# Kernel tuning notes

Hardware: AMD Instinct MI355X
Metric: run time of the kernel (lower is better)

## Reference

```python
import jax, jax.numpy as jnp
import numpy as np

H = 1024   # hidden_size
S = 1024   # seq_length
B = 32     # batch_size


def setup_inputs() -> dict:
    key = jax.random.key(0)
    k1, k2, k3, k4, k5, k6 = jax.random.split(key, 6)
    scale = 1.0 / np.sqrt(3 * H)
    return {
        "encoder_states": jax.random.normal(k1, (S, B, 2 * H), dtype=jnp.float32),
        "hidden": jax.random.normal(k2, (B, H), dtype=jnp.float32),
        "cell": jax.random.normal(k3, (B, H), dtype=jnp.float32),
        "W_attn": jax.random.normal(k4, (H, 3 * H), dtype=jnp.float32) * scale,
        "b_attn": jax.random.normal(k5, (H,), dtype=jnp.float32) * scale,
        "v_w": jax.random.normal(k6, (H,), dtype=jnp.float32) * (1.0 / np.sqrt(H)),
    }


def reference(encoder_states, hidden, cell, W_attn, b_attn, v_w):
    # cell is accepted by the original forward but unused.
    # Split the concat-linear into two projections (mathematically identical,
    # avoids materializing the repeated hidden + concat tensor):
    # cat((hidden_rep, enc), -1) @ W.T == hidden @ W[:, :H].T + enc @ W[:, H:].T
    W_h = W_attn[:, :H]          # [H, H]   multiplies decoder hidden
    W_e = W_attn[:, H:]          # [H, 2H]  multiplies encoder states
    enc = jnp.transpose(encoder_states, (1, 0, 2))          # [B, S, 2H]
    h_proj = hidden @ W_h.T + b_attn                         # [B, H], broadcast over S
    e_proj = jnp.einsum("bse,he->bsh", enc, W_e)             # [B, S, H]
    energy = jnp.tanh(h_proj[:, None, :] + e_proj)           # [B, S, H]
    attention = jnp.einsum("bsh,h->bs", energy, v_w)         # [B, S]
    return jax.nn.softmax(attention, axis=1)
```

## Files before the change

### kernel.cpp

```cpp
#include <hip/hip_runtime.h>
#include <hip/hip_bf16.h>

#define H 1024
#define S 1024
#define B 32
#define K2 2048

typedef unsigned short u16;
typedef __attribute__((ext_vector_type(8))) short short8;
typedef __attribute__((ext_vector_type(8))) unsigned short u16x8;
typedef __attribute__((ext_vector_type(4))) float floatx4;

__device__ __forceinline__ u16 f2bf(float f) {
  unsigned u = __float_as_uint(f);
  u += 0x7FFFu + ((u >> 16) & 1u);
  return (u16)(u >> 16);
}

__device__ __forceinline__ void gld_lds16(const void* g, void* l) {
  __builtin_amdgcn_global_load_lds(
      (const __attribute__((address_space(1))) unsigned int*)g,
      (__attribute__((address_space(3))) unsigned int*)l, 16, 0, 0);
}

__device__ __forceinline__ unsigned cvt_pk(float lo, float hi) {
  __hip_bfloat162 h = __float22bfloat162_rn(float2{lo, hi});
  return *(unsigned*)&h;
}

__device__ __forceinline__ short8 mk_frag(floatx4 lo, floatx4 hi) {
  union { unsigned u[4]; short8 s; } r;
  r.u[0] = cvt_pk(lo[0], lo[1]);
  r.u[1] = cvt_pk(lo[2], lo[3]);
  r.u[2] = cvt_pk(hi[0], hi[1]);
  r.u[3] = cvt_pk(hi[2], hi[3]);
  return r.s;
}

__global__ void conv_we_k(const float* __restrict__ W, u16* __restrict__ dst) {
  const int h = blockIdx.x;
  const int t = threadIdx.x * 8;
  const float* sp = W + (size_t)h * 3072 + H + t;
  u16* dp = dst + (size_t)h * K2 + t;
  floatx4 x = *(const floatx4*)sp;
  floatx4 y = *(const floatx4*)(sp + 4);
  u16x8 o;
  o[0] = f2bf(x[0]); o[1] = f2bf(x[1]); o[2] = f2bf(x[2]); o[3] = f2bf(x[3]);
  o[4] = f2bf(y[0]); o[5] = f2bf(y[1]); o[6] = f2bf(y[2]); o[7] = f2bf(y[3]);
  *(u16x8*)dp = o;
}

__global__ void hproj_k(const float* __restrict__ hidden, const float* __restrict__ W,
                        const float* __restrict__ b_attn, float* __restrict__ hp) {
  const int lane = threadIdx.x & 63;
  const int h = (blockIdx.x * blockDim.x + threadIdx.x) >> 6;
  float wr[16];
#pragma unroll
  for (int i = 0; i < 16; i++) wr[i] = W[(size_t)h * 3072 + lane + i * 64];
  for (int b = 0; b < B; b++) {
    float d = 0.f;
#pragma unroll
    for (int i = 0; i < 16; i++) d = fmaf(wr[i], hidden[b * H + lane + i * 64], d);
#pragma unroll
    for (int off = 32; off; off >>= 1) d += __shfl_xor(d, off);
    if (lane == 0) hp[b * H + h] = d + b_attn[h];
  }
}

#define BM 128
#define BN 128
#define BK 32

__global__ __launch_bounds__(256) void gemm_fused_k(
    const float* __restrict__ enc,
    const u16* __restrict__ Bw,
    const float* __restrict__ hp, const float* __restrict__ vw,
    float* __restrict__ attn) {
  __shared__ __align__(16) float sA[BM * 32];
  __shared__ __align__(16) u16 sB[BN * BK];
  const int tid = threadIdx.x;
  const int bid = blockIdx.x;
  const int ntile = bid >> 8;
  const int b = (bid & 255) >> 3;
  const int mtile = bid & 7;
  const int s0 = mtile * BM;
  const int h0 = ntile * BN;

  const int lane = tid & 63;
  const int wv = tid >> 6;
  const int wm = (wv >> 1) * 64;
  const int wn = (wv & 1) * 64;
  const int fr = lane & 15;
  const int kgrp = lane >> 4;

  const int lr8 = lane >> 3, sg8 = lane & 7;
  const int lr4 = lane >> 2, sg4 = lane & 3;

  floatx4 acc[4][4];
#pragma unroll
  for (int i = 0; i < 4; i++)
#pragma unroll
    for (int j = 0; j < 4; j++) acc[i][j] = (floatx4){0.f, 0.f, 0.f, 0.f};

  for (int k0 = 0; k0 < K2; k0 += BK) {
    __syncthreads();
#pragma unroll
    for (int p = 0; p < 4; p++) {
      const int r = wv * 32 + p * 8 + lr8;
      gld_lds16(enc + ((size_t)(s0 + r) * B + b) * K2 + k0 + ((sg8 ^ (r & 7)) << 2),
                (char*)sA + (wv * 32 + p * 8) * 128);
    }
#pragma unroll
    for (int p = 0; p < 2; p++) {
      const int r = wv * 32 + p * 16 + lr4;
      gld_lds16(Bw + (size_t)(h0 + r) * K2 + k0 + ((sg4 ^ ((r >> 1) & 3)) << 3),
                (char*)sB + (wv * 32 + p * 16) * 64);
    }
    __syncthreads();

    short8 af[4], bf[4];
#pragma unroll
    for (int mf = 0; mf < 4; mf++) {
      const int R = wm + mf * 16 + fr;
      const int f7 = R & 7;
      floatx4 lo = *(const floatx4*)&sA[R * 32 + ((((kgrp << 1)) ^ f7) << 2)];
      floatx4 hi = *(const floatx4*)&sA[R * 32 + ((((kgrp << 1) | 1) ^ f7) << 2)];
      af[mf] = mk_frag(lo, hi);
    }
#pragma unroll
    for (int nf = 0; nf < 4; nf++) {
      const int R = wn + nf * 16 + fr;
      bf[nf] = *(const short8*)&sB[R * BK + ((kgrp ^ ((R >> 1) & 3)) << 3)];
    }
#pragma unroll
    for (int mf = 0; mf < 4; mf++)
#pragma unroll
      for (int nf = 0; nf < 4; nf++)
        acc[mf][nf] =
            __builtin_amdgcn_mfma_f32_16x16x32_bf16(af[mf], bf[nf], acc[mf][nf], 0, 0, 0);
  }

  const int col = fr;
  const int rgrp = lane >> 4;
  float hv[4], vv[4];
#pragma unroll
  for (int nf = 0; nf < 4; nf++) {
    const int h = h0 + wn + nf * 16 + col;
    hv[nf] = hp[b * H + h];
    vv[nf] = vw[h];
  }
#pragma unroll
  for (int mf = 0; mf < 4; mf++) {
#pragma unroll
    for (int r = 0; r < 4; r++) {
      float part = 0.f;
#pragma unroll
      for (int nf = 0; nf < 4; nf++) part += tanhf(acc[mf][nf][r] + hv[nf]) * vv[nf];
      part += __shfl_xor(part, 1);
      part += __shfl_xor(part, 2);
      part += __shfl_xor(part, 4);
      part += __shfl_xor(part, 8);
      if (col == 0)
        atomicAdd(&attn[b * S + s0 + wm + mf * 16 + rgrp * 4 + r], part);
    }
  }
}

__global__ void softmax_k(const float* __restrict__ attn, float* __restrict__ out) {
  __shared__ float red[8];
  const int b = blockIdx.x;
  const int tid = threadIdx.x;
  const float* row = attn + b * S;
  float v[4];
#pragma unroll
  for (int i = 0; i < 4; i++) v[i] = row[tid + i * 256];
  float m = fmaxf(fmaxf(v[0], v[1]), fmaxf(v[2], v[3]));
#pragma unroll
  for (int off = 32; off; off >>= 1) m = fmaxf(m, __shfl_xor(m, off));
  if ((tid & 63) == 0) red[tid >> 6] = m;
  __syncthreads();
  m = fmaxf(fmaxf(red[0], red[1]), fmaxf(red[2], red[3]));
  float e[4], sum = 0.f;
#pragma unroll
  for (int i = 0; i < 4; i++) { e[i] = __expf(v[i] - m); sum += e[i]; }
#pragma unroll
  for (int off = 32; off; off >>= 1) sum += __shfl_xor(sum, off);
  __syncthreads();
  if ((tid & 63) == 0) red[4 + (tid >> 6)] = sum;
  __syncthreads();
  sum = red[4] + red[5] + red[6] + red[7];
  const float inv = 1.0f / sum;
#pragma unroll
  for (int i = 0; i < 4; i++) out[b * S + tid + i * 256] = e[i] * inv;
}

extern "C" void kernel_launch(void* const* d_in, const int* in_sizes, int n_in,
                              void* d_out, int out_size, void* d_ws, size_t ws_size,
                              hipStream_t stream) {
  const float* enc    = (const float*)d_in[0];
  const float* hidden = (const float*)d_in[1];
  const float* W_attn = (const float*)d_in[3];
  const float* b_attn = (const float*)d_in[4];
  const float* v_w    = (const float*)d_in[5];
  float* out = (float*)d_out;

  char* ws = (char*)d_ws;
  float* attn = (float*)ws;
  float* hp   = (float*)(ws + 131072);
  u16* Web    = (u16*)(ws + 262144);

  hipMemsetAsync(attn, 0, B * S * sizeof(float), stream);
  conv_we_k<<<H, 256, 0, stream>>>(W_attn, Web);
  hproj_k<<<256, 256, 0, stream>>>(hidden, W_attn, b_attn, hp);
  gemm_fused_k<<<2048, 256, 0, stream>>>(enc, Web, hp, v_w, attn);
  softmax_k<<<B, 256, 0, stream>>>(attn, out);
}
```

Before: 608.7 us.

## Pre-convert encoder states to transposed bf16 before the fused GEMM

Adds a pass that converts the fp32 encoder states into a bf16 buffer laid out as [B,S,2H], and a GEMM variant that loads bf16 A tiles straight into LDS with no per-tile fp32-to-bf16 packing. The GEMM's A-operand traffic is halved and the conversion work in the inner loop goes away. In exchange there is an extra full read of the 256MB fp32 input plus a 128MB write. The new path runs only when the workspace is large enough, otherwise the old kernel is used.

```diff
diff --git a/kernel.cpp b/kernel.cpp
--- a/kernel.cpp
+++ b/kernel.cpp
@@ -50,6 +50,21 @@
   *(u16x8*)dp = o;
 }
 
+__global__ void conv_enc_k(const float* __restrict__ enc, u16* __restrict__ dst) {
+  const int sb = blockIdx.x;
+  const int s = sb >> 5;
+  const int b = sb & 31;
+  const int t = threadIdx.x * 8;
+  const float* sp = enc + (size_t)sb * K2 + t;
+  u16* dp = dst + ((size_t)b * S + s) * K2 + t;
+  floatx4 x = *(const floatx4*)sp;
+  floatx4 y = *(const floatx4*)(sp + 4);
+  u16x8 o;
+  o[0] = f2bf(x[0]); o[1] = f2bf(x[1]); o[2] = f2bf(x[2]); o[3] = f2bf(x[3]);
+  o[4] = f2bf(y[0]); o[5] = f2bf(y[1]); o[6] = f2bf(y[2]); o[7] = f2bf(y[3]);
+  *(u16x8*)dp = o;
+}
+
 __global__ void hproj_k(const float* __restrict__ hidden, const float* __restrict__ W,
                         const float* __restrict__ b_attn, float* __restrict__ hp) {
   const int lane = threadIdx.x & 63;
@@ -70,6 +85,95 @@
 #define BM 128
 #define BN 128
 #define BK 32
+
+__global__ __launch_bounds__(256) void gemm_bf16_k(
+    const u16* __restrict__ A,
+    const u16* __restrict__ Bw,
+    const float* __restrict__ hp, const float* __restrict__ vw,
+    float* __restrict__ attn) {
+  __shared__ __align__(16) u16 sA[BM * BK];
+  __shared__ __align__(16) u16 sB[BN * BK];
+  const int tid = threadIdx.x;
+  const int bid = blockIdx.x;
+  const int ntile = bid >> 8;
+  const int b = (bid & 255) >> 3;
+  const int mtile = bid & 7;
+  const int s0 = mtile * BM;
+  const int h0 = ntile * BN;
+
+  const int lane = tid & 63;
+  const int wv = tid >> 6;
+  const int wm = (wv >> 1) * 64;
+  const int wn = (wv & 1) * 64;
+  const int fr = lane & 15;
+  const int kgrp = lane >> 4;
+
+  const int lr4 = lane >> 2, sg4 = lane & 3;
+
+  const u16* Abase = A + (size_t)b * S * K2;
+
+  floatx4 acc[4][4];
+#pragma unroll
+  for (int i = 0; i < 4; i++)
+#pragma unroll
+    for (int j = 0; j < 4; j++) acc[i][j] = (floatx4){0.f, 0.f, 0.f, 0.f};
+
+  for (int k0 = 0; k0 < K2; k0 += BK) {
+    __syncthreads();
+#pragma unroll
+    for (int p = 0; p < 2; p++) {
+      const int r = wv * 32 + p * 16 + lr4;
+      gld_lds16(Abase + (size_t)(s0 + r) * K2 + k0 + ((sg4 ^ ((r >> 1) & 3)) << 3),
+                (char*)sA + (wv * 32 + p * 16) * 64);
+      gld_lds16(Bw + (size_t)(h0 + r) * K2 + k0 + ((sg4 ^ ((r >> 1) & 3)) << 3),
+                (char*)sB + (wv * 32 + p * 16) * 64);
+    }
+    __syncthreads();
+
+    short8 af[4], bfr[4];
+#pragma unroll
+    for (int mf = 0; mf < 4; mf++) {
+      const int R = wm + mf * 16 + fr;
+      af[mf] = *(const short8*)&sA[R * BK + ((kgrp ^ ((R >> 1) & 3)) << 3)];
+    }
+#pragma unroll
+    for (int nf = 0; nf < 4; nf++) {
+      const int R = wn + nf * 16 + fr;
+      bfr[nf] = *(const short8*)&sB[R * BK + ((kgrp ^ ((R >> 1) & 3)) << 3)];
+    }
+#pragma unroll
+    for (int mf = 0; mf < 4; mf++)
+#pragma unroll
+      for (int nf = 0; nf < 4; nf++)
+        acc[mf][nf] =
+            __builtin_amdgcn_mfma_f32_16x16x32_bf16(af[mf], bfr[nf], acc[mf][nf], 0, 0, 0);
+  }
+
+  const int col = fr;
+  const int rgrp = lane >> 4;
+  float hv[4], vv[4];
+#pragma unroll
+  for (int nf = 0; nf < 4; nf++) {
+    const int h = h0 + wn + nf * 16 + col;
+    hv[nf] = hp[b * H + h];
+    vv[nf] = vw[h];
+  }
+#pragma unroll
+  for (int mf = 0; mf < 4; mf++) {
+#pragma unroll
+    for (int r = 0; r < 4; r++) {
+      float part = 0.f;
+#pragma unroll
+      for (int nf = 0; nf < 4; nf++) part += tanhf(acc[mf][nf][r] + hv[nf]) * vv[nf];
+      part += __shfl_xor(part, 1);
+      part += __shfl_xor(part, 2);
+      part += __shfl_xor(part, 4);
+      part += __shfl_xor(part, 8);
+      if (col == 0)
+        atomicAdd(&attn[b * S + s0 + wm + mf * 16 + rgrp * 4 + r], part);
+    }
+  }
+}
 
 __global__ __launch_bounds__(256) void gemm_fused_k(
     const float* __restrict__ enc,
@@ -118,7 +222,7 @@
     }
     __syncthreads();
 
-    short8 af[4], bf[4];
+    short8 af[4], bfr[4];
 #pragma unroll
     for (int mf = 0; mf < 4; mf++) {
       const int R = wm + mf * 16 + fr;
@@ -130,14 +234,14 @@
 #pragma unroll
     for (int nf = 0; nf < 4; nf++) {
       const int R = wn + nf * 16 + fr;
-      bf[nf] = *(const short8*)&sB[R * BK + ((kgrp ^ ((R >> 1) & 3)) << 3)];
+      bfr[nf] = *(const short8*)&sB[R * BK + ((kgrp ^ ((R >> 1) & 3)) << 3)];
     }
 #pragma unroll
     for (int mf = 0; mf < 4; mf++)
 #pragma unroll
       for (int nf = 0; nf < 4; nf++)
         acc[mf][nf] =
-            __builtin_amdgcn_mfma_f32_16x16x32_bf16(af[mf], bf[nf], acc[mf][nf], 0, 0, 0);
+            __builtin_amdgcn_mfma_f32_16x16x32_bf16(af[mf], bfr[nf], acc[mf][nf], 0, 0, 0);
   }
 
   const int col = fr;
@@ -208,10 +312,17 @@
   float* attn = (float*)ws;
   float* hp   = (float*)(ws + 131072);
   u16* Web    = (u16*)(ws + 262144);
+  u16* encb   = (u16*)(ws + 4456448);
+  const size_t need = 4456448 + (size_t)B * S * K2 * 2;
 
   hipMemsetAsync(attn, 0, B * S * sizeof(float), stream);
   conv_we_k<<<H, 256, 0, stream>>>(W_attn, Web);
   hproj_k<<<256, 256, 0, stream>>>(hidden, W_attn, b_attn, hp);
-  gemm_fused_k<<<2048, 256, 0, stream>>>(enc, Web, hp, v_w, attn);
+  if (ws_size >= need) {
+    conv_enc_k<<<S * B, 256, 0, stream>>>(enc, encb);
+    gemm_bf16_k<<<2048, 256, 0, stream>>>(encb, Web, hp, v_w, attn);
+  } else {
+    gemm_fused_k<<<2048, 256, 0, stream>>>(enc, Web, hp, v_w, attn);
+  }
   softmax_k<<<B, 256, 0, stream>>>(attn, out);
 }
```

Measured after the change: 614.9 us. No clear change (+1.0%).

## Double-buffer GEMM tiles and convert encoder to bf16 once at LDS store

Applied to the files above, without the earlier changes.

The GEMM main loop now uses two LDS buffers. Encoder fp32 data for the next K-step is loaded into registers and the weight tile is prefetched asynchronously while MFMAs run on the current buffer, leaving one barrier per iteration instead of two. Encoder data is converted to bf16 once per element when written to LDS, not on every fragment read, which also halves LDS size and read traffic for A. The cost is more registers for prefetched data, a launch_bounds occupancy hint, and the A load no longer going directly from global to LDS.

```diff
diff --git a/kernel.cpp b/kernel.cpp
--- a/kernel.cpp
+++ b/kernel.cpp
@@ -71,13 +71,13 @@
 #define BN 128
 #define BK 32
 
-__global__ __launch_bounds__(256) void gemm_fused_k(
+__global__ __launch_bounds__(256, 4) void gemm_fused2_k(
     const float* __restrict__ enc,
     const u16* __restrict__ Bw,
     const float* __restrict__ hp, const float* __restrict__ vw,
     float* __restrict__ attn) {
-  __shared__ __align__(16) float sA[BM * 32];
-  __shared__ __align__(16) u16 sB[BN * BK];
+  __shared__ __align__(16) u16 sA[2][BM * BK];
+  __shared__ __align__(16) u16 sB[2][BN * BK];
   const int tid = threadIdx.x;
   const int bid = blockIdx.x;
   const int ntile = bid >> 8;
@@ -93,7 +93,13 @@
   const int fr = lane & 15;
   const int kgrp = lane >> 4;
 
-  const int lr8 = lane >> 3, sg8 = lane & 7;
+  const int ar = tid >> 1;
+  const int ah = tid & 1;
+  const int asw = (ar >> 1) & 3;
+  const float* agp = enc + ((size_t)(s0 + ar) * B + b) * K2 + ah * 16;
+  const int aseg0 = ((2 * ah) ^ asw) << 3;
+  const int aseg1 = ((2 * ah + 1) ^ asw) << 3;
+
   const int lr4 = lane >> 2, sg4 = lane & 3;
 
   floatx4 acc[4][4];
@@ -102,42 +108,64 @@
 #pragma unroll
     for (int j = 0; j < 4; j++) acc[i][j] = (floatx4){0.f, 0.f, 0.f, 0.f};
 
-  for (int k0 = 0; k0 < K2; k0 += BK) {
-    __syncthreads();
-#pragma unroll
-    for (int p = 0; p < 4; p++) {
-      const int r = wv * 32 + p * 8 + lr8;
-      gld_lds16(enc + ((size_t)(s0 + r) * B + b) * K2 + k0 + ((sg8 ^ (r & 7)) << 2),
-                (char*)sA + (wv * 32 + p * 8) * 128);
-    }
-#pragma unroll
-    for (int p = 0; p < 2; p++) {
-      const int r = wv * 32 + p * 16 + lr4;
-      gld_lds16(Bw + (size_t)(h0 + r) * K2 + k0 + ((sg4 ^ ((r >> 1) & 3)) << 3),
-                (char*)sB + (wv * 32 + p * 16) * 64);
-    }
-    __syncthreads();
-
-    short8 af[4], bf[4];
+  floatx4 a0, a1, a2, a3;
+
+  a0 = *(const floatx4*)(agp + 0);
+  a1 = *(const floatx4*)(agp + 4);
+  a2 = *(const floatx4*)(agp + 8);
+  a3 = *(const floatx4*)(agp + 12);
+#pragma unroll
+  for (int p = 0; p < 2; p++) {
+    const int r = wv * 32 + p * 16 + lr4;
+    gld_lds16(Bw + (size_t)(h0 + r) * K2 + ((sg4 ^ ((r >> 1) & 3)) << 3),
+              (char*)sB[0] + (wv * 32 + p * 16) * 64);
+  }
+  {
+    u16* aw = &sA[0][ar * BK];
+    *(short8*)(aw + aseg0) = mk_frag(a0, a1);
+    *(short8*)(aw + aseg1) = mk_frag(a2, a3);
+  }
+  __syncthreads();
+
+  for (int t = 0; t < K2 / BK; ++t) {
+    const int c = t & 1;
+    const int k1 = (t + 1) * BK;
+    if (k1 < K2) {
+      const float* ap = agp + k1;
+      a0 = *(const floatx4*)(ap + 0);
+      a1 = *(const floatx4*)(ap + 4);
+      a2 = *(const floatx4*)(ap + 8);
+      a3 = *(const floatx4*)(ap + 12);
+#pragma unroll
+      for (int p = 0; p < 2; p++) {
+        const int r = wv * 32 + p * 16 + lr4;
+        gld_lds16(Bw + (size_t)(h0 + r) * K2 + k1 + ((sg4 ^ ((r >> 1) & 3)) << 3),
+                  (char*)sB[1 - c] + (wv * 32 + p * 16) * 64);
+      }
+    }
+    short8 af[4], bfr[4];
 #pragma unroll
     for (int mf = 0; mf < 4; mf++) {
       const int R = wm + mf * 16 + fr;
-      const int f7 = R & 7;
-      floatx4 lo = *(const floatx4*)&sA[R * 32 + ((((kgrp << 1)) ^ f7) << 2)];
-      floatx4 hi = *(const floatx4*)&sA[R * 32 + ((((kgrp << 1) | 1) ^ f7) << 2)];
-      af[mf] = mk_frag(lo, hi);
+      af[mf] = *(const short8*)&sA[c][R * BK + ((kgrp ^ ((R >> 1) & 3)) << 3)];
     }
 #pragma unroll
     for (int nf = 0; nf < 4; nf++) {
       const int R = wn + nf * 16 + fr;
-      bf[nf] = *(const short8*)&sB[R * BK + ((kgrp ^ ((R >> 1) & 3)) << 3)];
+      bfr[nf] = *(const short8*)&sB[c][R * BK + ((kgrp ^ ((R >> 1) & 3)) << 3)];
     }
 #pragma unroll
     for (int mf = 0; mf < 4; mf++)
 #pragma unroll
       for (int nf = 0; nf < 4; nf++)
         acc[mf][nf] =
-            __builtin_amdgcn_mfma_f32_16x16x32_bf16(af[mf], bf[nf], acc[mf][nf], 0, 0, 0);
+            __builtin_amdgcn_mfma_f32_16x16x32_bf16(af[mf], bfr[nf], acc[mf][nf], 0, 0, 0);
+    if (k1 < K2) {
+      u16* aw = &sA[1 - c][ar * BK];
+      *(short8*)(aw + aseg0) = mk_frag(a0, a1);
+      *(short8*)(aw + aseg1) = mk_frag(a2, a3);
+    }
+    __syncthreads();
   }
 
   const int col = fr;
@@ -212,6 +240,6 @@
   hipMemsetAsync(attn, 0, B * S * sizeof(float), stream);
   conv_we_k<<<H, 256, 0, stream>>>(W_attn, Web);
   hproj_k<<<256, 256, 0, stream>>>(hidden, W_attn, b_attn, hp);
-  gemm_fused_k<<<2048, 256, 0, stream>>>(enc, Web, hp, v_w, attn);
+  gemm_fused2_k<<<2048, 256, 0, stream>>>(enc, Web, hp, v_w, attn);
   softmax_k<<<B, 256, 0, stream>>>(attn, out);
 }
```

Result: no change. 620.3 us (+1.9%).
